# Optimization experiments

Measured on AMD Instinct MI355X. Metric: run time of the kernel, lower is better.

The kernel has to match this reference:

```python
import jax, jax.numpy as jnp
import numpy as np

EMBED_DIM = 1024
NUM_HEADS = 16
HEAD_DIM = EMBED_DIM // NUM_HEADS


def setup_inputs() -> dict:
    key = jax.random.key(0)
    ks = jax.random.split(key, 9)
    s = 1.0 / np.sqrt(EMBED_DIM)
    X = jax.random.normal(ks[0], (4, 2048, EMBED_DIM), dtype=jnp.float32)
    # Linear weights stored as [in, out] for x @ W + b
    Wq = jax.random.uniform(ks[1], (EMBED_DIM, EMBED_DIM), jnp.float32, -s, s)
    bq = jax.random.uniform(ks[2], (EMBED_DIM,), jnp.float32, -s, s)
    Wk = jax.random.uniform(ks[3], (EMBED_DIM, EMBED_DIM), jnp.float32, -s, s)
    bk = jax.random.uniform(ks[4], (EMBED_DIM,), jnp.float32, -s, s)
    Wv = jax.random.uniform(ks[5], (EMBED_DIM, EMBED_DIM), jnp.float32, -s, s)
    bv = jax.random.uniform(ks[6], (EMBED_DIM,), jnp.float32, -s, s)
    Wo = jax.random.uniform(ks[7], (EMBED_DIM, EMBED_DIM), jnp.float32, -s, s)
    bo = jax.random.uniform(ks[8], (EMBED_DIM,), jnp.float32, -s, s)
    return {"X": X, "Wq": Wq, "bq": bq, "Wk": Wk, "bk": bk,
            "Wv": Wv, "bv": bv, "Wo": Wo, "bo": bo}


def reference(X, Wq, bq, Wk, bk, Wv, bv, Wo, bo):
    B, S, _ = X.shape
    def split_heads(t):  # [B,S,E] -> [B,H,S,D]
        return t.reshape(B, S, NUM_HEADS, HEAD_DIM).transpose(0, 2, 1, 3)
    Q = split_heads(X @ Wq + bq)
    K = split_heads(X @ Wk + bk)
    V = split_heads(X @ Wv + bv)
    scale = 1.0 / np.sqrt(HEAD_DIM).astype(np.float32)
    scores = jnp.einsum('bhqd,bhkd->bhqk', Q, K) * scale
    probs = jax.nn.softmax(scores, axis=-1)
    attn = jnp.einsum('bhqk,bhkd->bhqd', probs, V)  # [B,H,S,D]
    combined = attn.transpose(0, 2, 1, 3).reshape(B, S, EMBED_DIM)
    return combined @ Wo + bo
```

## Files before the change

### kernel.cpp

```cpp
#include <hip/hip_runtime.h>
#include <hip/hip_bf16.h>

#define EMBED 1024
#define NHEADS 16
#define HDIM 64
#define SEQ 2048
#define BATCH 4
#define ROWS (BATCH * SEQ)

typedef __attribute__((ext_vector_type(8))) short bf16x8;
typedef __attribute__((ext_vector_type(4))) short short4v;
typedef __attribute__((ext_vector_type(4))) float f32x4;
typedef __attribute__((ext_vector_type(2))) float f32x2;
typedef __attribute__((ext_vector_type(16))) float f32x16;
typedef __attribute__((ext_vector_type(4))) unsigned int u32x4;
typedef __attribute__((ext_vector_type(2))) unsigned int u32x2;
typedef __attribute__((ext_vector_type(2))) int i32x2;
typedef unsigned int u32;

#define SL2E 0.18033688011112042f

__device__ __forceinline__ short f2bf(float f) {
    u32 u = __builtin_bit_cast(u32, f) + 0x8000u;
    return (short)(u >> 16);
}

__device__ __forceinline__ u32 pkbf(float a, float b) {
    u32 ua = __builtin_bit_cast(u32, a) + 0x8000u;
    u32 ub = __builtin_bit_cast(u32, b) + 0x8000u;
    return __builtin_amdgcn_perm(ua, ub, 0x03020706u);
}

__device__ __forceinline__ float fexp2(float x) {
#if __has_builtin(__builtin_amdgcn_exp2f)
    return __builtin_amdgcn_exp2f(x);
#else
    return exp2f(x);
#endif
}

__device__ __forceinline__ void async16(const void* g, void* l) {
    __builtin_amdgcn_global_load_lds((const __attribute__((address_space(1))) u32*)g,
                                     (__attribute__((address_space(3))) u32*)l, 16, 0, 0);
}

__global__ __launch_bounds__(256) void convert_f32_bf16(const float* __restrict__ in,
                                                        short* __restrict__ out) {
    int i = (blockIdx.x * 256 + threadIdx.x) * 4;
    float4 v = *(const float4*)&in[i];
    u32x2 o = { pkbf(v.x, v.y), pkbf(v.z, v.w) };
    *(u32x2*)&out[i] = o;
}

__global__ __launch_bounds__(256) void transpose_w4(const float* __restrict__ W0,
                                                    const float* __restrict__ W1,
                                                    const float* __restrict__ W2,
                                                    const float* __restrict__ W3,
                                                    short* __restrict__ T0,
                                                    short* __restrict__ T1,
                                                    short* __restrict__ T2,
                                                    short* __restrict__ T3) {
    const int z = blockIdx.z;
    const float* W = (z == 0) ? W0 : (z == 1) ? W1 : (z == 2) ? W2 : W3;
    short* WT = (z == 0) ? T0 : (z == 1) ? T1 : (z == 2) ? T2 : T3;
    const float sc = (z == 0) ? SL2E : 1.0f;
    __shared__ float T[64][65];
    const int k0 = blockIdx.y * 64, n0 = blockIdx.x * 64;
    const int rr = threadIdx.x >> 4, cc = (threadIdx.x & 15) * 4;
    #pragma unroll
    for (int p = 0; p < 4; ++p) {
        int r = p * 16 + rr;
        float4 v = *(const float4*)&W[(size_t)(k0 + r) * EMBED + n0 + cc];
        T[r][cc] = v.x * sc; T[r][cc + 1] = v.y * sc; T[r][cc + 2] = v.z * sc; T[r][cc + 3] = v.w * sc;
    }
    __syncthreads();
    #pragma unroll
    for (int p = 0; p < 4; ++p) {
        int r = p * 16 + rr;
        u32x2 o = { pkbf(T[cc][r], T[cc + 1][r]), pkbf(T[cc + 2][r], T[cc + 3][r]) };
        *(u32x2*)&WT[(size_t)(n0 + r) * EMBED + k0 + cc] = o;
    }
}

__global__ __launch_bounds__(256, 5) void gemm_bf16_128(const short* __restrict__ A,
                                                        const short* __restrict__ BT0,
                                                        const short* __restrict__ BT1,
                                                        const short* __restrict__ BT2,
                                                        const float* __restrict__ b0,
                                                        const float* __restrict__ b1,
                                                        const float* __restrict__ b2,
                                                        void* __restrict__ C0,
                                                        void* __restrict__ C1,
                                                        void* __restrict__ C2,
                                                        int mode) {
    const int z = blockIdx.z;
    const short* BT = (z == 0) ? BT0 : (z == 1) ? BT1 : BT2;
    const float* bias = (z == 0) ? b0 : (z == 1) ? b1 : b2;
    const float bsc = (mode == 0 && z == 0) ? SL2E : 1.0f;
    __shared__ short As[128 * 64];
    __shared__ short Bs[64 * 64];
    const int tid = threadIdx.x;
    const int wave = tid >> 6, lane = tid & 63;
    const int c = lane & 15, quad = lane >> 4;
    const int sw = c & 7;
    const int row0 = blockIdx.y * 128, col0 = blockIdx.x * 64;
    f32x4 acc[2][4] = {};
    for (int k0 = 0; k0 < EMBED; k0 += 64) {
        #pragma unroll
        for (int it = 0; it < 4; ++it) {
            int ci = (it * 4 + wave) * 64 + lane;
            int row = ci >> 3, g = (ci & 7) ^ (row & 7);
            async16(&A[(size_t)(row0 + row) * EMBED + k0 + g * 8], &As[(it * 4 + wave) * 512]);
        }
        #pragma unroll
        for (int it = 0; it < 2; ++it) {
            int ci = (it * 4 + wave) * 64 + lane;
            int row = ci >> 3, g = (ci & 7) ^ (row & 7);
            async16(&BT[(size_t)(col0 + row) * EMBED + k0 + g * 8], &Bs[(it * 4 + wave) * 512]);
        }
        __syncthreads();
        #pragma unroll
        for (int ks = 0; ks < 2; ++ks) {
            bf16x8 af[2], bfr[4];
            #pragma unroll
            for (int i = 0; i < 2; ++i)
                af[i] = *(const bf16x8*)&As[(wave * 32 + i * 16 + c) * 64 + ((ks * 4 + quad) ^ sw) * 8];
            #pragma unroll
            for (int j = 0; j < 4; ++j)
                bfr[j] = *(const bf16x8*)&Bs[(j * 16 + c) * 64 + ((ks * 4 + quad) ^ sw) * 8];
            #pragma unroll
            for (int i = 0; i < 2; ++i)
                #pragma unroll
                for (int j = 0; j < 4; ++j)
                    acc[i][j] = __builtin_amdgcn_mfma_f32_16x16x32_bf16(af[i], bfr[j], acc[i][j], 0, 0, 0);
        }
        __syncthreads();
    }
    if (mode == 0 && z == 2) {
        short* Vt = (short*)C2;
        const int b = row0 >> 11, s0 = (row0 & 2047) + wave * 32;
        const int bh = b * NHEADS + blockIdx.x;
        #pragma unroll
        for (int i = 0; i < 2; ++i)
            #pragma unroll
            for (int j = 0; j < 4; ++j) {
                int d = j * 16 + c;
                float bv = bias[col0 + d];
                int s = s0 + i * 16 + quad * 4;
                u32x2 o = { pkbf(acc[i][j][0] + bv, acc[i][j][1] + bv),
                            pkbf(acc[i][j][2] + bv, acc[i][j][3] + bv) };
                *(u32x2*)&Vt[((size_t)bh * HDIM + d) * SEQ + s] = o;
            }
    } else {
        void* Cout = (z == 0) ? C0 : (z == 1) ? C1 : C2;
        #pragma unroll
        for (int i = 0; i < 2; ++i)
            #pragma unroll
            for (int j = 0; j < 4; ++j) {
                int colb = col0 + j * 16 + c;
                float bv = bias[colb] * bsc;
                #pragma unroll
                for (int r = 0; r < 4; ++r) {
                    int row = row0 + wave * 32 + i * 16 + quad * 4 + r;
                    float v = acc[i][j][r] + bv;
                    if (mode == 0) ((short*)Cout)[(size_t)row * EMBED + colb] = f2bf(v);
                    else           ((float*)Cout)[(size_t)row * EMBED + colb] = v;
                }
            }
    }
}

__global__ __launch_bounds__(256, 3) void attn_mfma(const short* __restrict__ Qb,
                                                    const short* __restrict__ Kb,
                                                    const short* __restrict__ Vt,
                                                    short* __restrict__ Ob) {
    __shared__ short SH[8192];
    short* Ks = SH;
    short* Vs = SH + 4096;
    const int tid = threadIdx.x;
    const int wave = tid >> 6, lane = tid & 63;
    const int l31 = lane & 31, h = lane >> 5;
    const int swz = l31 & 7;
    const int bh = blockIdx.y;
    const int b = bh >> 4, hd = bh & 15;
    const size_t base = (size_t)b * SEQ * EMBED + (size_t)hd * HDIM;
    const size_t vbase = (size_t)bh * HDIM * SEQ;
    const int q0 = blockIdx.x * 128;

    bf16x8 qf[4];
    #pragma unroll
    for (int ks = 0; ks < 4; ++ks)
        qf[ks] = *(const bf16x8*)&Qb[base + (size_t)(q0 + wave * 32 + l31) * EMBED + ks * 16 + h * 8];

    const short* kp[2];
    const short* vp[2];
    int ldofs[2];
    #pragma unroll
    for (int it = 0; it < 2; ++it) {
        int ci = (it * 4 + wave) * 64 + lane;
        int row = ci >> 3, g = (ci & 7) ^ (row & 7);
        kp[it] = Kb + base + (size_t)row * EMBED + g * 8;
        vp[it] = Vt + vbase + (size_t)row * SEQ + g * 8;
        ldofs[it] = (it * 4 + wave) * 512;
    }

    f32x16 O[2] = {};
    f32x2 ls = {0.0f, 0.0f};

    for (int kt = 0; kt < SEQ / 64; ++kt) {
        #pragma unroll
        for (int it = 0; it < 2; ++it) {
            async16(kp[it], &Ks[ldofs[it]]);
            async16(vp[it], &Vs[ldofs[it]]);
            kp[it] += 64 * EMBED;
            vp[it] += 64;
        }
        __syncthreads();

        f32x16 st[2] = {};
        #pragma unroll
        for (int nt = 0; nt < 2; ++nt)
            #pragma unroll
            for (int ks = 0; ks < 4; ++ks) {
                bf16x8 ak = *(const bf16x8*)&Ks[(nt * 32 + l31) * 64 + ((ks * 2 + h) ^ swz) * 8];
                st[nt] = __builtin_amdgcn_mfma_f32_32x32x16_bf16(ak, qf[ks], st[nt], 0, 0, 0);
            }

        u32 pk[2][8];
        #pragma unroll
        for (int nt = 0; nt < 2; ++nt)
            #pragma unroll
            for (int i = 0; i < 8; ++i) {
                float e0 = fexp2(st[nt][2 * i]), e1 = fexp2(st[nt][2 * i + 1]);
                f32x2 e = { e0, e1 };
                ls += e;
                pk[nt][i] = pkbf(e0, e1);
            }

        #pragma unroll
        for (int ks = 0; ks < 4; ++ks) {
            const int nt = ks >> 1, bs = (ks & 1) * 4;
            u32x4 fr;
#if __has_builtin(__builtin_amdgcn_permlane32_swap)
            i32x2 sA = __builtin_amdgcn_permlane32_swap((int)pk[nt][bs + 0], (int)pk[nt][bs + 2], false, false);
            i32x2 sB = __builtin_amdgcn_permlane32_swap((int)pk[nt][bs + 1], (int)pk[nt][bs + 3], false, false);
            fr.x = (u32)sA.x; fr.y = (u32)sB.x; fr.z = (u32)sA.y; fr.w = (u32)sB.y;
#else
            u32 s0 = h ? pk[nt][bs + 0] : pk[nt][bs + 2];
            u32 s1 = h ? pk[nt][bs + 1] : pk[nt][bs + 3];
            u32 r0 = (u32)__shfl_xor((int)s0, 32);
            u32 r1 = (u32)__shfl_xor((int)s1, 32);
            fr.x = h ? r0 : pk[nt][bs + 0];
            fr.y = h ? r1 : pk[nt][bs + 1];
            fr.z = h ? pk[nt][bs + 2] : r0;
            fr.w = h ? pk[nt][bs + 3] : r1;
#endif
            bf16x8 pf = __builtin_bit_cast(bf16x8, fr);
            #pragma unroll
            for (int mt = 0; mt < 2; ++mt) {
                bf16x8 vf = *(const bf16x8*)&Vs[(mt * 32 + l31) * 64 + ((ks * 2 + h) ^ swz) * 8];
                O[mt] = __builtin_amdgcn_mfma_f32_32x32x16_bf16(vf, pf, O[mt], 0, 0, 0);
            }
        }
        __syncthreads();
    }

    float lsum = ls.x + ls.y;
    lsum += __shfl_xor(lsum, 32);
    float inv = 1.0f / lsum;

    const int wbase = wave * 2048;
    #pragma unroll
    for (int mt = 0; mt < 2; ++mt)
        #pragma unroll
        for (int m = 0; m < 4; ++m) {
            u32x2 wv;
            wv.x = pkbf(O[mt][4 * m + 0] * inv, O[mt][4 * m + 1] * inv);
            wv.y = pkbf(O[mt][4 * m + 2] * inv, O[mt][4 * m + 3] * inv);
            int u = mt * 8 + 2 * m + h;
            int su = u ^ ((l31 & 7) << 1);
            *(u32x2*)&SH[wbase + l31 * 64 + su * 4] = wv;
        }
    __syncthreads();
    #pragma unroll
    for (int p = 0; p < 4; ++p) {
        int ci = p * 256 + tid;
        int wq = ci >> 8, rem = ci & 255;
        int r = rem >> 3, cch = rem & 7;
        int su = (2 * cch) ^ ((r & 7) << 1);
        bf16x8 val = *(const bf16x8*)&SH[wq * 2048 + r * 64 + su * 4];
        *(bf16x8*)&Ob[base + (size_t)(q0 + wq * 32 + r) * EMBED + cch * 8] = val;
    }
}

extern "C" void kernel_launch(void* const* d_in, const int* in_sizes, int n_in,
                              void* d_out, int out_size, void* d_ws, size_t ws_size,
                              hipStream_t stream)
{
    const float* X  = (const float*)d_in[0];
    const float* Wq = (const float*)d_in[1];
    const float* bq = (const float*)d_in[2];
    const float* Wk = (const float*)d_in[3];
    const float* bk = (const float*)d_in[4];
    const float* Wv = (const float*)d_in[5];
    const float* bv = (const float*)d_in[6];
    const float* Wo = (const float*)d_in[7];
    const float* bo = (const float*)d_in[8];
    float* out = (float*)d_out;

    const size_t NE = (size_t)ROWS * EMBED;
    short* Xbf = (short*)d_ws;
    short* Qb  = Xbf + NE;
    short* Kb  = Qb + NE;
    short* Vtb = Kb + NE;
    short* WqT = Vtb + NE;
    short* WkT = WqT + (size_t)EMBED * EMBED;
    short* WvT = WkT + (size_t)EMBED * EMBED;
    short* WoT = WvT + (size_t)EMBED * EMBED;

    convert_f32_bf16<<<(ROWS * EMBED) / 1024, 256, 0, stream>>>(X, Xbf);
    dim3 gw(16, 16, 4);
    transpose_w4<<<gw, 256, 0, stream>>>(Wq, Wk, Wv, Wo, WqT, WkT, WvT, WoT);

    dim3 gq(EMBED / 64, ROWS / 128, 3);
    gemm_bf16_128<<<gq, 256, 0, stream>>>(Xbf, WqT, WkT, WvT, bq, bk, bv,
                                          Qb, Kb, Vtb, 0);

    dim3 gt(SEQ / 128, BATCH * NHEADS);
    attn_mfma<<<gt, 256, 0, stream>>>(Qb, Kb, Vtb, Qb);

    dim3 gg(EMBED / 64, ROWS / 128, 1);
    gemm_bf16_128<<<gg, 256, 0, stream>>>(Qb, WoT, WoT, WoT, bo, bo, bo,
                                          out, out, out, 1);
}
```

Baseline: 280.7 us.

## Replace projection GEMMs with 256x256 double-buffered pipelined bf16 GEMM

Replaces the 128x64 single-buffered GEMM with a 256x256-tile, 512-thread kernel. It double-buffers LDS, interleaves async global-to-LDS staging with MFMA phases, and uses setprio and fine-grained waitcnt/barriers. The QKV projection now treats WqT/WkT/WvT as one contiguous 3072-wide weight matrix, and the output block decides z from the column index. The larger tiles improve data reuse and hide load latency. The cost is heavy register and LDS pressure (128 KB shared), and it relies on the transposed weights being laid out contiguously in the workspace.

```diff
diff --git a/kernel.cpp b/kernel.cpp
--- a/kernel.cpp
+++ b/kernel.cpp
@@ -9,7 +9,6 @@
 #define ROWS (BATCH * SEQ)
 
 typedef __attribute__((ext_vector_type(8))) short bf16x8;
-typedef __attribute__((ext_vector_type(4))) short short4v;
 typedef __attribute__((ext_vector_type(4))) float f32x4;
 typedef __attribute__((ext_vector_type(2))) float f32x2;
 typedef __attribute__((ext_vector_type(16))) float f32x16;
@@ -82,92 +81,153 @@
     }
 }
 
-__global__ __launch_bounds__(256, 5) void gemm_bf16_128(const short* __restrict__ A,
-                                                        const short* __restrict__ BT0,
-                                                        const short* __restrict__ BT1,
-                                                        const short* __restrict__ BT2,
-                                                        const float* __restrict__ b0,
-                                                        const float* __restrict__ b1,
-                                                        const float* __restrict__ b2,
-                                                        void* __restrict__ C0,
-                                                        void* __restrict__ C1,
-                                                        void* __restrict__ C2,
-                                                        int mode) {
-    const int z = blockIdx.z;
-    const short* BT = (z == 0) ? BT0 : (z == 1) ? BT1 : BT2;
-    const float* bias = (z == 0) ? b0 : (z == 1) ? b1 : b2;
-    const float bsc = (mode == 0 && z == 0) ? SL2E : 1.0f;
-    __shared__ short As[128 * 64];
-    __shared__ short Bs[64 * 64];
+__global__ __launch_bounds__(512, 2) void gemm256(const short* __restrict__ A,
+                                                  const short* __restrict__ BT,
+                                                  const float* __restrict__ b0,
+                                                  const float* __restrict__ b1,
+                                                  const float* __restrict__ b2,
+                                                  void* __restrict__ C0,
+                                                  void* __restrict__ C1,
+                                                  void* __restrict__ C2,
+                                                  int mode) {
+    __shared__ short As[2][16384];
+    __shared__ short Bs[2][16384];
     const int tid = threadIdx.x;
-    const int wave = tid >> 6, lane = tid & 63;
-    const int c = lane & 15, quad = lane >> 4;
-    const int sw = c & 7;
-    const int row0 = blockIdx.y * 128, col0 = blockIdx.x * 64;
-    f32x4 acc[2][4] = {};
-    for (int k0 = 0; k0 < EMBED; k0 += 64) {
-        #pragma unroll
-        for (int it = 0; it < 4; ++it) {
-            int ci = (it * 4 + wave) * 64 + lane;
-            int row = ci >> 3, g = (ci & 7) ^ (row & 7);
-            async16(&A[(size_t)(row0 + row) * EMBED + k0 + g * 8], &As[(it * 4 + wave) * 512]);
-        }
-        #pragma unroll
-        for (int it = 0; it < 2; ++it) {
-            int ci = (it * 4 + wave) * 64 + lane;
-            int row = ci >> 3, g = (ci & 7) ^ (row & 7);
-            async16(&BT[(size_t)(col0 + row) * EMBED + k0 + g * 8], &Bs[(it * 4 + wave) * 512]);
-        }
-        __syncthreads();
-        #pragma unroll
-        for (int ks = 0; ks < 2; ++ks) {
-            bf16x8 af[2], bfr[4];
-            #pragma unroll
-            for (int i = 0; i < 2; ++i)
-                af[i] = *(const bf16x8*)&As[(wave * 32 + i * 16 + c) * 64 + ((ks * 4 + quad) ^ sw) * 8];
-            #pragma unroll
-            for (int j = 0; j < 4; ++j)
-                bfr[j] = *(const bf16x8*)&Bs[(j * 16 + c) * 64 + ((ks * 4 + quad) ^ sw) * 8];
-            #pragma unroll
-            for (int i = 0; i < 2; ++i)
+    const int wid = tid >> 6, lane = tid & 63;
+    const int c16 = lane & 15, quad = lane >> 4, sw = c16 & 7;
+    const int wm = wid >> 2, wn = wid & 3;
+    const int rowblk = blockIdx.y * 256, colblk = blockIdx.x * 256;
+
+    const int r0 = tid >> 3;
+    const int g0 = (tid & 7) ^ (r0 & 7);
+    const short* aS0 = A + (size_t)(rowblk + r0) * EMBED + g0 * 8;
+    const short* bS0 = BT + (size_t)(colblk + r0) * EMBED + g0 * 8;
+
+#define STAGE_A(SBUF, H, V) do { \
+    const short* _s = aS0 + (size_t)(H) * 131072 + (V) * 64; \
+    async16(_s,         &As[SBUF][(H) * 8192 + wid * 512]); \
+    async16(_s + 65536, &As[SBUF][(H) * 8192 + wid * 512 + 4096]); \
+} while (0)
+#define STAGE_B(SBUF, H, V) do { \
+    const short* _s = bS0 + (size_t)(H) * 131072 + (V) * 64; \
+    async16(_s,         &Bs[SBUF][(H) * 8192 + wid * 512]); \
+    async16(_s + 65536, &Bs[SBUF][(H) * 8192 + wid * 512 + 4096]); \
+} while (0)
+
+    f32x4 acc[8][4] = {};
+
+#define PHASE(BUF, MH, NH, SAB, SBUF, SH, SV, VM) do { \
+    bf16x8 af[4][2], bfv[2][2]; \
+    _Pragma("unroll") \
+    for (int fm = 0; fm < 4; ++fm) { \
+        const int row = (MH) * 128 + wm * 64 + fm * 16 + c16; \
+        _Pragma("unroll") \
+        for (int ks = 0; ks < 2; ++ks) \
+            af[fm][ks] = *(const bf16x8*)&As[BUF][row * 64 + ((ks * 4 + quad) ^ sw) * 8]; \
+    } \
+    _Pragma("unroll") \
+    for (int fn = 0; fn < 2; ++fn) { \
+        const int rowb = (NH) * 128 + wn * 32 + fn * 16 + c16; \
+        _Pragma("unroll") \
+        for (int ks = 0; ks < 2; ++ks) \
+            bfv[fn][ks] = *(const bf16x8*)&Bs[BUF][rowb * 64 + ((ks * 4 + quad) ^ sw) * 8]; \
+    } \
+    if ((SAB) == 0) STAGE_A(SBUF, SH, SV); else STAGE_B(SBUF, SH, SV); \
+    __builtin_amdgcn_s_barrier(); \
+    asm volatile("s_waitcnt lgkmcnt(0)" ::: "memory"); \
+    __builtin_amdgcn_s_setprio(1); \
+    _Pragma("unroll") \
+    for (int fm = 0; fm < 4; ++fm) \
+        _Pragma("unroll") \
+        for (int fn = 0; fn < 2; ++fn) \
+            _Pragma("unroll") \
+            for (int ks = 0; ks < 2; ++ks) \
+                acc[(MH) * 4 + fm][(NH) * 2 + fn] = \
+                    __builtin_amdgcn_mfma_f32_16x16x32_bf16(af[fm][ks], bfv[fn][ks], \
+                        acc[(MH) * 4 + fm][(NH) * 2 + fn], 0, 0, 0); \
+    __builtin_amdgcn_s_setprio(0); \
+    if (VM) asm volatile("s_waitcnt vmcnt(4)" ::: "memory"); \
+    __builtin_amdgcn_s_barrier(); \
+} while (0)
+
+    STAGE_A(0, 0, 0); STAGE_B(0, 0, 0);
+    STAGE_A(0, 1, 0); STAGE_B(0, 1, 0);
+    STAGE_A(1, 0, 1); STAGE_B(1, 0, 1);
+    asm volatile("s_waitcnt vmcnt(4)" ::: "memory");
+    __builtin_amdgcn_s_barrier();
+
+    #pragma unroll 1
+    for (int it = 0; it < 8; ++it) {
+        const int u = 2 * it;
+        const int v1 = u + 1, v2 = (u + 2) & 15, v3 = (u + 3) & 15;
+        PHASE(0, 0, 0, 0, 1, 1, v1, 0);
+        PHASE(0, 0, 1, 1, 1, 1, v1, 0);
+        PHASE(0, 1, 0, 0, 0, 0, v2, 0);
+        PHASE(0, 1, 1, 1, 0, 0, v2, 1);
+        PHASE(1, 0, 0, 0, 0, 1, v2, 0);
+        PHASE(1, 0, 1, 1, 0, 1, v2, 0);
+        PHASE(1, 1, 0, 0, 1, 0, v3, 0);
+        PHASE(1, 1, 1, 1, 1, 0, v3, 1);
+    }
+
+    asm volatile("s_waitcnt vmcnt(0)" ::: "memory");
+
+    const int rb0 = rowblk + wm * 64 + quad * 4;
+    const int cb0 = wn * 32 + c16;
+    if (mode == 0) {
+        const int z = colblk >> 10;
+        const int cm = colblk & 1023;
+        const float* bias = (z == 0) ? b0 : (z == 1) ? b1 : b2;
+        if (z == 2) {
+            short* Vt = (short*)C2;
+            #pragma unroll
+            for (int m = 0; m < 8; ++m) {
+                const int row = rb0 + (m >> 2) * 128 + (m & 3) * 16;
+                const int b = row >> 11, s = row & 2047;
                 #pragma unroll
-                for (int j = 0; j < 4; ++j)
-                    acc[i][j] = __builtin_amdgcn_mfma_f32_16x16x32_bf16(af[i], bfr[j], acc[i][j], 0, 0, 0);
-        }
-        __syncthreads();
-    }
-    if (mode == 0 && z == 2) {
-        short* Vt = (short*)C2;
-        const int b = row0 >> 11, s0 = (row0 & 2047) + wave * 32;
-        const int bh = b * NHEADS + blockIdx.x;
-        #pragma unroll
-        for (int i = 0; i < 2; ++i)
-            #pragma unroll
-            for (int j = 0; j < 4; ++j) {
-                int d = j * 16 + c;
-                float bv = bias[col0 + d];
-                int s = s0 + i * 16 + quad * 4;
-                u32x2 o = { pkbf(acc[i][j][0] + bv, acc[i][j][1] + bv),
-                            pkbf(acc[i][j][2] + bv, acc[i][j][3] + bv) };
-                *(u32x2*)&Vt[((size_t)bh * HDIM + d) * SEQ + s] = o;
-            }
+                for (int n = 0; n < 4; ++n) {
+                    const int cv = cm + cb0 + (n >> 1) * 128 + (n & 1) * 16;
+                    const int head = cv >> 6, d = cv & 63;
+                    const float bv = bias[cv];
+                    u32x2 o = { pkbf(acc[m][n][0] + bv, acc[m][n][1] + bv),
+                                pkbf(acc[m][n][2] + bv, acc[m][n][3] + bv) };
+                    *(u32x2*)&Vt[((size_t)(b * NHEADS + head) * HDIM + d) * SEQ + s] = o;
+                }
+            }
+        } else {
+            short* Cq = (short*)((z == 0) ? C0 : C1);
+            const float bsc = (z == 0) ? SL2E : 1.0f;
+            #pragma unroll
+            for (int m = 0; m < 8; ++m) {
+                const int row = rb0 + (m >> 2) * 128 + (m & 3) * 16;
+                #pragma unroll
+                for (int n = 0; n < 4; ++n) {
+                    const int col = cm + cb0 + (n >> 1) * 128 + (n & 1) * 16;
+                    const float bv = bias[col] * bsc;
+                    #pragma unroll
+                    for (int r = 0; r < 4; ++r)
+                        Cq[(size_t)(row + r) * EMBED + col] = f2bf(acc[m][n][r] + bv);
+                }
+            }
+        }
     } else {
-        void* Cout = (z == 0) ? C0 : (z == 1) ? C1 : C2;
-        #pragma unroll
-        for (int i = 0; i < 2; ++i)
-            #pragma unroll
-            for (int j = 0; j < 4; ++j) {
-                int colb = col0 + j * 16 + c;
-                float bv = bias[colb] * bsc;
+        float* Co = (float*)C0;
+        #pragma unroll
+        for (int m = 0; m < 8; ++m) {
+            const int row = rb0 + (m >> 2) * 128 + (m & 3) * 16;
+            #pragma unroll
+            for (int n = 0; n < 4; ++n) {
+                const int col = colblk + cb0 + (n >> 1) * 128 + (n & 1) * 16;
+                const float bv = b0[col];
                 #pragma unroll
-                for (int r = 0; r < 4; ++r) {
-                    int row = row0 + wave * 32 + i * 16 + quad * 4 + r;
-                    float v = acc[i][j][r] + bv;
-                    if (mode == 0) ((short*)Cout)[(size_t)row * EMBED + colb] = f2bf(v);
-                    else           ((float*)Cout)[(size_t)row * EMBED + colb] = v;
-                }
-            }
-    }
+                for (int r = 0; r < 4; ++r)
+                    Co[(size_t)(row + r) * EMBED + col] = acc[m][n][r] + bv;
+            }
+        }
+    }
+#undef PHASE
+#undef STAGE_A
+#undef STAGE_B
 }
 
 __global__ __launch_bounds__(256, 3) void attn_mfma(const short* __restrict__ Qb,
@@ -322,14 +382,12 @@
     dim3 gw(16, 16, 4);
     transpose_w4<<<gw, 256, 0, stream>>>(Wq, Wk, Wv, Wo, WqT, WkT, WvT, WoT);
 
-    dim3 gq(EMBED / 64, ROWS / 128, 3);
-    gemm_bf16_128<<<gq, 256, 0, stream>>>(Xbf, WqT, WkT, WvT, bq, bk, bv,
-                                          Qb, Kb, Vtb, 0);
+    dim3 gq(12, 32, 1);
+    gemm256<<<gq, 512, 0, stream>>>(Xbf, WqT, bq, bk, bv, Qb, Kb, Vtb, 0);
 
     dim3 gt(SEQ / 128, BATCH * NHEADS);
     attn_mfma<<<gt, 256, 0, stream>>>(Qb, Kb, Vtb, Qb);
 
-    dim3 gg(EMBED / 64, ROWS / 128, 1);
-    gemm_bf16_128<<<gg, 256, 0, stream>>>(Qb, WoT, WoT, WoT, bo, bo, bo,
-                                          out, out, out, 1);
-}
+    dim3 gg(4, 32, 1);
+    gemm256<<<gg, 512, 0, stream>>>(Qb, WoT, bo, bo, bo, out, out, out, 1);
+}
```

Measured after the change: 311.3 us. 1.11x slower.
